# Optimization experiments

Hardware: AMD Instinct MI355X
Metric: run time of the kernel (lower is better)

The kernel has to match this reference:

```python
import jax, jax.numpy as jnp
import numpy as np

BETA = 0.25


def setup_inputs() -> dict:
    key = jax.random.key(0)
    k1, k2 = jax.random.split(key)
    inp = jax.random.normal(k1, (8, 64, 64, 64), dtype=jnp.float32)   # [B,C,H,W]
    book = jax.random.normal(k2, (8192, 64), dtype=jnp.float32)       # [K,D], D==C
    return {"input": inp, "book": book}


def reference(input, book):
    # Faithful translation of the original forward (including its quirks:
    # the cross term is summed to a SCALAR, and z_q is viewed back into
    # input.shape (NCHW) before permute(0,3,1,2) -> [B,W,C,H]).
    B, C, H, W = input.shape
    D = book.shape[1]  # == C
    z = jnp.transpose(input, (0, 2, 3, 1)).reshape(-1, D)          # [N, D]
    # scalar cross term: sum_{n,k} z_n . e_k == (sum_n z_n) . (sum_k e_k)
    cross = jnp.dot(jnp.sum(z, axis=0), jnp.sum(book, axis=0))
    d = (jnp.sum(z * z, axis=1, keepdims=True)                     # [N,1]
         + jnp.sum(book * book, axis=1)                            # [K]  -> broadcast [N,K]
         - 2.0 * cross)
    idx = jnp.argmin(d, axis=1)                                     # [N]
    z_q = book[idx].reshape(input.shape)                            # raw reshape to [B,C,H,W]
    loss = (jnp.mean((jax.lax.stop_gradient(z_q) - input) ** 2)
            + BETA * jnp.mean((z_q - jax.lax.stop_gradient(input)) ** 2))
    z_q = jnp.transpose(z_q, (0, 3, 1, 2))                          # [B,W,C,H] as in source
    return (z_q, idx, loss)
```

## Files before the change

kernel.cpp:

```cpp
#include <hip/hip_runtime.h>


#define NTOT    2097152
#define NIDX    32768
#define K_ROWS  8192
#define K1_BLK  512
#define K2_BLK  512
#define K2_ITER 4


__global__ __launch_bounds__(256) void k1_argmin(const float* __restrict__ book,
                                                 unsigned long long* __restrict__ ws_keys) {
    const int t   = threadIdx.x;
    const int rIn = t >> 4;
    const int c4  = t & 15;
    const int row = blockIdx.x * 16 + rIn;

    const float4 v = ((const float4*)book)[row * 16 + c4];
    float s = v.x * v.x + v.y * v.y + v.z * v.z + v.w * v.w;
    s += __shfl_down(s, 8, 16);
    s += __shfl_down(s, 4, 16);
    s += __shfl_down(s, 2, 16);
    s += __shfl_down(s, 1, 16);

    __shared__ unsigned long long keys[16];
    if (c4 == 0) {
        keys[rIn] = ((unsigned long long)__float_as_uint(s) << 32)
                  | (unsigned int)row;
    }
    __syncthreads();
    if (t == 0) {
        unsigned long long k = keys[0];
        #pragma unroll
        for (int i = 1; i < 16; ++i) k = keys[i] < k ? keys[i] : k;
        ws_keys[blockIdx.x] = k;
    }
}

__global__ __launch_bounds__(256) void k2_main(const float* __restrict__ in,
                                               const float* __restrict__ book,
                                               float* __restrict__ out,
                                               const unsigned long long* __restrict__ ws_keys,
                                               float* __restrict__ ws_part) {
    const int lane = threadIdx.x & 63, wid = threadIdx.x >> 6;

    __shared__ unsigned long long skey;
    if (wid == 0) {
        unsigned long long key = ~0ULL;
        #pragma unroll
        for (int j = 0; j < K1_BLK / 64; ++j) {
            unsigned long long o = ws_keys[lane + j * 64];
            key = o < key ? o : key;
        }
        #pragma unroll
        for (int off = 32; off > 0; off >>= 1) {
            unsigned long long o = __shfl_down(key, off, 64);
            key = o < key ? o : key;
        }
        if (lane == 0) skey = key;
    }
    __syncthreads();
    const int kmin = (int)(skey & 0xFFFFFFFFu);
    const float* __restrict__ e = book + kmin * 64;

    const int tid = blockIdx.x * 256 + threadIdx.x;

    if (tid < NIDX / 4) {
        const float kf = (float)kmin;
        ((float4*)(out + NTOT))[tid] = make_float4(kf, kf, kf, kf);
    }

    float part = 0.f;
    #pragma unroll
    for (int it = 0; it < K2_ITER; ++it) {
        const int i = tid + it * (K2_BLK * 256);
        const float ev = e[(i >> 10) & 63];
        ((float4*)out)[i] = make_float4(ev, ev, ev, ev);
        const float4 z  = ((const float4*)in)[i];
        const float4 ef = ((const float4*)e)[i & 15];
        const float d0 = z.x - ef.x, d1 = z.y - ef.y;
        const float d2 = z.z - ef.z, d3 = z.w - ef.w;
        part += d0 * d0 + d1 * d1 + d2 * d2 + d3 * d3;
    }
    #pragma unroll
    for (int off = 32; off > 0; off >>= 1) part += __shfl_down(part, off, 64);

    __shared__ float sp[4];
    if (lane == 0) sp[wid] = part;
    __syncthreads();
    if (threadIdx.x == 0)
        ws_part[blockIdx.x] = sp[0] + sp[1] + sp[2] + sp[3];
}

__global__ __launch_bounds__(64) void k3_loss(const float* __restrict__ ws_part,
                                              float* __restrict__ out) {
    float s = 0.f;
    #pragma unroll
    for (int j = 0; j < K2_BLK / 64; ++j) s += ws_part[threadIdx.x + j * 64];
    #pragma unroll
    for (int off = 32; off > 0; off >>= 1) s += __shfl_down(s, off, 64);
    if (threadIdx.x == 0)
        out[NTOT + NIDX] = s * (1.25f / (float)NTOT);
}

extern "C" void kernel_launch(void* const* d_in, const int* in_sizes, int n_in,
                              void* d_out, int out_size, void* d_ws, size_t ws_size,
                              hipStream_t stream) {
    const float* in   = (const float*)d_in[0];
    const float* book = (const float*)d_in[1];
    float* out = (float*)d_out;

    unsigned long long* ws_keys = (unsigned long long*)d_ws;
    float*              ws_part = (float*)((char*)d_ws + 4096);

    k1_argmin<<<K1_BLK, 256, 0, stream>>>(book, ws_keys);
    k2_main<<<K2_BLK, 256, 0, stream>>>(in, book, out, ws_keys, ws_part);
    k3_loss<<<1, 64, 0, stream>>>(ws_part, out);
}
```

Measured before the change: 67.58 us.

## Expand loss algebraically and move input reduction into the argmin kernel

The input reads move into the first kernel, overlapping them with the codebook norm scan. That kernel now produces per-block sums of z and z^2 per channel position. The loss is expanded as sum z^2 - 2 sum z·e + N·|e|^2, so the second kernel only writes outputs, and block 0 finishes the loss in double precision. This removes the third kernel launch and the serial dependency between reading the input and finding the argmin. In exchange, block 0 of the second kernel does extra serial reduction work.

```diff
diff --git a/kernel.cpp b/kernel.cpp
--- a/kernel.cpp
+++ b/kernel.cpp
@@ -1,23 +1,30 @@
 #include <hip/hip_runtime.h>
 
 
-#define NTOT    2097152
-#define NIDX    32768
-#define K_ROWS  8192
-#define K1_BLK  512
-#define K2_BLK  512
-#define K2_ITER 4
+#define NTOT  2097152
+#define NIDX  32768
+#define NBLK  512
 
 
-__global__ __launch_bounds__(256) void k1_argmin(const float* __restrict__ book,
-                                                 unsigned long long* __restrict__ ws_keys) {
-    const int t   = threadIdx.x;
-    const int rIn = t >> 4;
+__global__ __launch_bounds__(256) void kA(const float* __restrict__ in,
+                                          const float* __restrict__ book,
+                                          unsigned long long* __restrict__ ws_keys,
+                                          float* __restrict__ ws_sin2,
+                                          float4* __restrict__ ws_S) {
+    const int t    = threadIdx.x;
+    const int b    = blockIdx.x;
+    const int lane = t & 63, wid = t >> 6;
+
+    const int row = b * 16 + (t >> 4);
     const int c4  = t & 15;
-    const int row = blockIdx.x * 16 + rIn;
+    const float4 bv = ((const float4*)book)[row * 16 + c4];
 
-    const float4 v = ((const float4*)book)[row * 16 + c4];
-    float s = v.x * v.x + v.y * v.y + v.z * v.z + v.w * v.w;
+    float4 z[4];
+    #pragma unroll
+    for (int it = 0; it < 4; ++it)
+        z[it] = ((const float4*)in)[b * 256 + t + it * (NBLK * 256)];
+
+    float s = bv.x * bv.x + bv.y * bv.y + bv.z * bv.z + bv.w * bv.w;
     s += __shfl_down(s, 8, 16);
     s += __shfl_down(s, 4, 16);
     s += __shfl_down(s, 2, 16);
@@ -25,30 +32,61 @@
 
     __shared__ unsigned long long keys[16];
     if (c4 == 0) {
-        keys[rIn] = ((unsigned long long)__float_as_uint(s) << 32)
-                  | (unsigned int)row;
+        keys[t >> 4] = ((unsigned long long)__float_as_uint(s) << 32)
+                     | (unsigned int)row;
     }
+
+    float4 sv = make_float4(0.f, 0.f, 0.f, 0.f);
+    float  s2 = 0.f;
+    #pragma unroll
+    for (int it = 0; it < 4; ++it) {
+        sv.x += z[it].x; sv.y += z[it].y; sv.z += z[it].z; sv.w += z[it].w;
+        s2 += z[it].x * z[it].x + z[it].y * z[it].y
+            + z[it].z * z[it].z + z[it].w * z[it].w;
+    }
+    sv.x += __shfl_down(sv.x, 32, 64); sv.y += __shfl_down(sv.y, 32, 64);
+    sv.z += __shfl_down(sv.z, 32, 64); sv.w += __shfl_down(sv.w, 32, 64);
+    sv.x += __shfl_down(sv.x, 16, 64); sv.y += __shfl_down(sv.y, 16, 64);
+    sv.z += __shfl_down(sv.z, 16, 64); sv.w += __shfl_down(sv.w, 16, 64);
+    #pragma unroll
+    for (int off = 32; off > 0; off >>= 1) s2 += __shfl_down(s2, off, 64);
+
+    __shared__ float4 sWl[4][16];
+    __shared__ float  s2l[4];
+    if (lane < 16) sWl[wid][lane] = sv;
+    if (lane == 0) s2l[wid] = s2;
     __syncthreads();
+
     if (t == 0) {
         unsigned long long k = keys[0];
         #pragma unroll
         for (int i = 1; i < 16; ++i) k = keys[i] < k ? keys[i] : k;
-        ws_keys[blockIdx.x] = k;
+        ws_keys[b] = k;
     }
+    if (t < 16) {
+        float4 a = sWl[0][t], b4 = sWl[1][t], c = sWl[2][t], d = sWl[3][t];
+        ws_S[b * 16 + t] = make_float4(a.x + b4.x + c.x + d.x,
+                                       a.y + b4.y + c.y + d.y,
+                                       a.z + b4.z + c.z + d.z,
+                                       a.w + b4.w + c.w + d.w);
+    }
+    if (t == 16)
+        ws_sin2[b] = s2l[0] + s2l[1] + s2l[2] + s2l[3];
 }
 
-__global__ __launch_bounds__(256) void k2_main(const float* __restrict__ in,
-                                               const float* __restrict__ book,
-                                               float* __restrict__ out,
-                                               const unsigned long long* __restrict__ ws_keys,
-                                               float* __restrict__ ws_part) {
-    const int lane = threadIdx.x & 63, wid = threadIdx.x >> 6;
+__global__ __launch_bounds__(256) void kB(const float* __restrict__ book,
+                                          float* __restrict__ out,
+                                          const unsigned long long* __restrict__ ws_keys,
+                                          const float* __restrict__ ws_sin2,
+                                          const float4* __restrict__ ws_S) {
+    const int t    = threadIdx.x;
+    const int lane = t & 63, wid = t >> 6;
 
     __shared__ unsigned long long skey;
     if (wid == 0) {
         unsigned long long key = ~0ULL;
         #pragma unroll
-        for (int j = 0; j < K1_BLK / 64; ++j) {
+        for (int j = 0; j < NBLK / 64; ++j) {
             unsigned long long o = ws_keys[lane + j * 64];
             key = o < key ? o : key;
         }
@@ -63,44 +101,57 @@
     const int kmin = (int)(skey & 0xFFFFFFFFu);
     const float* __restrict__ e = book + kmin * 64;
 
-    const int tid = blockIdx.x * 256 + threadIdx.x;
+    const int tid = blockIdx.x * 256 + t;
 
     if (tid < NIDX / 4) {
         const float kf = (float)kmin;
         ((float4*)(out + NTOT))[tid] = make_float4(kf, kf, kf, kf);
     }
 
-    float part = 0.f;
     #pragma unroll
-    for (int it = 0; it < K2_ITER; ++it) {
-        const int i = tid + it * (K2_BLK * 256);
+    for (int it = 0; it < 4; ++it) {
+        const int i = tid + it * (NBLK * 256);
         const float ev = e[(i >> 10) & 63];
         ((float4*)out)[i] = make_float4(ev, ev, ev, ev);
-        const float4 z  = ((const float4*)in)[i];
-        const float4 ef = ((const float4*)e)[i & 15];
-        const float d0 = z.x - ef.x, d1 = z.y - ef.y;
-        const float d2 = z.z - ef.z, d3 = z.w - ef.w;
-        part += d0 * d0 + d1 * d1 + d2 * d2 + d3 * d3;
     }
-    #pragma unroll
-    for (int off = 32; off > 0; off >>= 1) part += __shfl_down(part, off, 64);
 
-    __shared__ float sp[4];
-    if (lane == 0) sp[wid] = part;
-    __syncthreads();
-    if (threadIdx.x == 0)
-        ws_part[blockIdx.x] = sp[0] + sp[1] + sp[2] + sp[3];
-}
-
-__global__ __launch_bounds__(64) void k3_loss(const float* __restrict__ ws_part,
-                                              float* __restrict__ out) {
-    float s = 0.f;
-    #pragma unroll
-    for (int j = 0; j < K2_BLK / 64; ++j) s += ws_part[threadIdx.x + j * 64];
-    #pragma unroll
-    for (int off = 32; off > 0; off >>= 1) s += __shfl_down(s, off, 64);
-    if (threadIdx.x == 0)
-        out[NTOT + NIDX] = s * (1.25f / (float)NTOT);
+    if (blockIdx.x == 0) {
+        double a2 = 0.0, aes = 0.0, ae2 = 0.0;
+        if (t < 16) {
+            const float4 ef = ((const float4*)e)[t];
+            ae2 = (double)ef.x * ef.x + (double)ef.y * ef.y
+                + (double)ef.z * ef.z + (double)ef.w * ef.w;
+        }
+        #pragma unroll
+        for (int h = 0; h < 2; ++h) {
+            const int blk = t + h * 256;
+            a2 += (double)ws_sin2[blk];
+            #pragma unroll
+            for (int j = 0; j < 16; ++j) {
+                const float4 sv = ws_S[blk * 16 + j];
+                const float4 ef = ((const float4*)e)[j];
+                aes += (double)sv.x * ef.x + (double)sv.y * ef.y
+                     + (double)sv.z * ef.z + (double)sv.w * ef.w;
+            }
+        }
+        #pragma unroll
+        for (int off = 32; off > 0; off >>= 1) {
+            a2  += __shfl_down(a2,  off, 64);
+            aes += __shfl_down(aes, off, 64);
+            ae2 += __shfl_down(ae2, off, 64);
+        }
+        __shared__ double sA[4], sE[4], sQ[4];
+        if (lane == 0) { sA[wid] = a2; sE[wid] = aes; sQ[wid] = ae2; }
+        __syncthreads();
+        if (t == 0) {
+            const double A2 = sA[0] + sA[1] + sA[2] + sA[3];
+            const double ES = sE[0] + sE[1] + sE[2] + sE[3];
+            const double E2 = sQ[0] + sQ[1] + sQ[2] + sQ[3];
+            const double loss = 1.25 * (A2 - 2.0 * ES + 32768.0 * E2)
+                              / (double)NTOT;
+            out[NTOT + NIDX] = (float)loss;
+        }
+    }
 }
 
 extern "C" void kernel_launch(void* const* d_in, const int* in_sizes, int n_in,
@@ -111,9 +162,9 @@
     float* out = (float*)d_out;
 
     unsigned long long* ws_keys = (unsigned long long*)d_ws;
-    float*              ws_part = (float*)((char*)d_ws + 4096);
+    float*              ws_sin2 = (float*)((char*)d_ws + 4096);
+    float4*             ws_S    = (float4*)((char*)d_ws + 8192);
 
-    k1_argmin<<<K1_BLK, 256, 0, stream>>>(book, ws_keys);
-    k2_main<<<K2_BLK, 256, 0, stream>>>(in, book, out, ws_keys, ws_part);
-    k3_loss<<<1, 64, 0, stream>>>(ws_part, out);
+    kA<<<NBLK, 256, 0, stream>>>(in, book, ws_keys, ws_sin2, ws_S);
+    kB<<<NBLK, 256, 0, stream>>>(book, out, ws_keys, ws_sin2, ws_S);
 }
```

Measured after the change: 72.93 us. +7.9%, slower.
